# Performance work log

Hardware: AMD Instinct MI355X
Metric: run time of the kernel (lower is better)

The kernel has to match this reference:

```python
import jax, jax.numpy as jnp
import numpy as np

B, W, H, V, L = 64, 512, 1024, 32000, 2


def setup_inputs() -> dict:
    key = jax.random.key(0)
    ks = jax.random.split(key, 20)
    s = 0.02  # init scale
    n = lambda k, shp: jax.random.normal(k, shp, jnp.float32)
    return {
        "input": jax.random.randint(ks[0], (B, 1), 0, V),
        "h0": n(ks[1], (L, B, H)),
        "c0": n(ks[2], (L, B, H)),
        "encoder_output": n(ks[3], (B, W, H)),
        "embedding": n(ks[4], (V, H)) * s,
        "W_ih0": n(ks[5], (4 * H, H)) * s,
        "W_hh0": n(ks[6], (4 * H, H)) * s,
        "b_ih0": n(ks[7], (4 * H,)) * s,
        "b_hh0": n(ks[8], (4 * H,)) * s,
        "W_ih1": n(ks[9], (4 * H, H)) * s,
        "W_hh1": n(ks[10], (4 * H, H)) * s,
        "b_ih1": n(ks[11], (4 * H,)) * s,
        "b_hh1": n(ks[12], (4 * H,)) * s,
        "att_w": n(ks[13], (2 * H,)) * s,
        "att_b": n(ks[14], (1,)) * s,
        "input_W": n(ks[15], (H, 2 * H)) * s,
        "input_b": n(ks[16], (H,)) * s,
        "out_W": n(ks[17], (V, H)) * s,
        "out_b": n(ks[18], (V,)) * s,
    }


def _lstm_step(x, h, c, W_ih, W_hh, b_ih, b_hh):
    # PyTorch gate order: i, f, g, o
    g = x @ W_ih.T + h @ W_hh.T + b_ih + b_hh
    i, f, gg, o = jnp.split(g, 4, axis=-1)
    c2 = jax.nn.sigmoid(f) * c + jax.nn.sigmoid(i) * jnp.tanh(gg)
    return jax.nn.sigmoid(o) * jnp.tanh(c2), c2


def reference(input, h0, c0, encoder_output, embedding,
              W_ih0, W_hh0, b_ih0, b_hh0, W_ih1, W_hh1, b_ih1, b_hh1,
              att_w, att_b, input_W, input_b, out_W, out_b):
    Hd = h0.shape[-1]
    emb = embedding[input]                       # (B,1,H)
    att_state = h0[-1] * c0[-1]                  # (B,H)
    # Vectorized replacement of the per-word cat+linear loop:
    # att_line(cat(enc_w, att_state)) = enc_w @ w_enc + att_state @ w_st + b
    w_enc, w_st = att_w[:Hd], att_w[Hd:]
    scores = encoder_output @ w_enc + (att_state @ w_st)[:, None] + att_b[0]  # (B,W)
    # Original quirk: weigth starts with a zeros column, then softmax over
    # weigth[:, 0:-1] -> zero column + scores for words 0..W-2 (last dropped).
    zeros = jnp.zeros((scores.shape[0], 1), scores.dtype)
    full = jnp.concatenate([zeros, scores[:, :-1]], axis=1)  # (B,W)
    wts = jax.nn.softmax(full, axis=1)
    ctx = jnp.einsum('bw,bwh->bh', wts, encoder_output)      # (B,H)
    x = jnp.concatenate([ctx, emb[:, 0, :]], axis=-1)        # (B,2H)
    x = x @ input_W.T + input_b                              # (B,H)
    h1, c1 = _lstm_step(x, h0[0], c0[0], W_ih0, W_hh0, b_ih0, b_hh0)
    h2, c2 = _lstm_step(h1, h0[1], c0[1], W_ih1, W_hh1, b_ih1, b_hh1)
    logits = h2 @ out_W.T + out_b                            # (B,V)
    logp = jax.nn.log_softmax(logits, axis=-1)[:, None, :]   # (B,1,V)
    return logp, jnp.stack([h1, h2]), jnp.stack([c1, c2])
```

## Files before the change

kernel.cpp:

```cpp
#include <hip/hip_runtime.h>
#include <hip/hip_bf16.h>

#define Bsz 64
#define Wln 512
#define Hd  1024
#define Vc  32000

typedef short v8s __attribute__((ext_vector_type(8)));
typedef float f32x4 __attribute__((ext_vector_type(4)));

__device__ inline unsigned short f2b(float f) {
  union { float f; unsigned u; } v; v.f = f;
  return (unsigned short)((v.u + 0x8000u) >> 16);
}
__device__ inline float b2f(unsigned short u) {
  union { float f; unsigned u; } v; v.u = ((unsigned)u) << 16; return v.f;
}
__device__ inline float wave_sum(float v) {
  #pragma unroll
  for (int o = 32; o; o >>= 1) v += __shfl_down(v, o);
  return v;
}
__device__ inline float wave_max(float v) {
  #pragma unroll
  for (int o = 32; o; o >>= 1) v = fmaxf(v, __shfl_down(v, o));
  return v;
}
__device__ inline float wave_sum_all(float v) {
  #pragma unroll
  for (int o = 32; o; o >>= 1) v += __shfl_xor(v, o);
  return v;
}
__device__ inline float wave_max_all(float v) {
  #pragma unroll
  for (int o = 32; o; o >>= 1) v = fmaxf(v, __shfl_xor(v, o));
  return v;
}
__device__ inline float sigm(float x) { return 1.f / (1.f + expf(-x)); }

__device__ inline v8s cvt_frag(float4 x0, float4 x1) {
  v8s r;
  r[0] = (short)f2b(x0.x); r[1] = (short)f2b(x0.y);
  r[2] = (short)f2b(x0.z); r[3] = (short)f2b(x0.w);
  r[4] = (short)f2b(x1.x); r[5] = (short)f2b(x1.y);
  r[6] = (short)f2b(x1.z); r[7] = (short)f2b(x1.w);
  return r;
}

__device__ inline void stage_A(const float* __restrict__ A, const float* __restrict__ Ab,
                               int sA, char* pool, int tid) {
  #pragma unroll
  for (int it = 0; it < 16; ++it) {
    int idx = it * 512 + tid;
    int row = idx >> 7, ch = idx & 127;
    const float* src = A + (size_t)row * sA + ch * 8;
    float4 x0 = *(const float4*)src;
    float4 x1 = *(const float4*)(src + 4);
    if (Ab) {
      const float* s2 = Ab + (size_t)row * sA + ch * 8;
      float4 y0 = *(const float4*)s2;
      float4 y1 = *(const float4*)(s2 + 4);
      x0.x += y0.x; x0.y += y0.y; x0.z += y0.z; x0.w += y0.w;
      x1.x += y1.x; x1.y += y1.y; x1.z += y1.z; x1.w += y1.w;
    }
    *(v8s*)(pool + row * 2048 + ((ch * 16) ^ ((row & 7) << 4))) = cvt_frag(x0, x1);
  }
}

__global__ __launch_bounds__(512, 4) void k_attn(
    const float* __restrict__ enc, const float* __restrict__ att_w,
    const float* __restrict__ h0, const float* __restrict__ c0,
    const float* __restrict__ att_b,
    ushort* __restrict__ ctxp, float* __restrict__ ps_a)
{
  __shared__ __align__(16) float pool[8 * 1024];
  __shared__ float dots[17];
  __shared__ float redA[8];
  __shared__ float wts_sh[16];
  const int b = blockIdx.x >> 5, ch = blockIdx.x & 31;
  const int c0r = ch * 16;
  const int tid = threadIdx.x, w = tid >> 6, lane = tid & 63;
  const float* encb = enc + (size_t)b * Wln * Hd;

  const float* r0p = encb + (size_t)(c0r + 2 * w) * Hd;
  const float* r1p = r0p + Hd;
  float4 e0[4], e1[4], aw[4];
  #pragma unroll
  for (int i = 0; i < 4; ++i) {
    e0[i] = *(const float4*)(r0p + (i * 64 + lane) * 4);
    e1[i] = *(const float4*)(r1p + (i * 64 + lane) * 4);
    aw[i] = *(const float4*)(att_w + (i * 64 + lane) * 4);
  }

  {
    size_t base = (size_t)(Bsz + b) * Hd;
    int j = tid * 2;
    float s = h0[base + j] * c0[base + j] * att_w[Hd + j]
            + h0[base + j + 1] * c0[base + j + 1] * att_w[Hd + j + 1];
    s = wave_sum(s);
    if (lane == 0) redA[w] = s;
  }

  {
    float s0 = e0[0].x*aw[0].x + e0[0].y*aw[0].y + e0[0].z*aw[0].z + e0[0].w*aw[0].w
             + e0[1].x*aw[1].x + e0[1].y*aw[1].y + e0[1].z*aw[1].z + e0[1].w*aw[1].w
             + e0[2].x*aw[2].x + e0[2].y*aw[2].y + e0[2].z*aw[2].z + e0[2].w*aw[2].w
             + e0[3].x*aw[3].x + e0[3].y*aw[3].y + e0[3].z*aw[3].z + e0[3].w*aw[3].w;
    float s1 = e1[0].x*aw[0].x + e1[0].y*aw[0].y + e1[0].z*aw[0].z + e1[0].w*aw[0].w
             + e1[1].x*aw[1].x + e1[1].y*aw[1].y + e1[1].z*aw[1].z + e1[1].w*aw[1].w
             + e1[2].x*aw[2].x + e1[2].y*aw[2].y + e1[2].z*aw[2].z + e1[2].w*aw[2].w
             + e1[3].x*aw[3].x + e1[3].y*aw[3].y + e1[3].z*aw[3].z + e1[3].w*aw[3].w;
    s0 = wave_sum(s0);
    s1 = wave_sum(s1);
    if (lane == 0) { dots[2 * w + 1] = s0; dots[2 * w + 2] = s1; }
  }
  if (w == 7 && c0r > 0) {
    const float* hp = encb + (size_t)(c0r - 1) * Hd;
    float s = 0.f;
    #pragma unroll
    for (int i = 0; i < 4; ++i) {
      float4 hv = *(const float4*)(hp + (i * 64 + lane) * 4);
      s += hv.x*aw[i].x + hv.y*aw[i].y + hv.z*aw[i].z + hv.w*aw[i].w;
    }
    s = wave_sum(s);
    if (lane == 0) dots[0] = s;
  }
  __syncthreads();

  float sa = att_b[0];
  #pragma unroll
  for (int i = 0; i < 8; ++i) sa += redA[i];

  int r0 = c0r + 2 * w;
  float wt0 = (r0 == 0) ? 1.f : expf(dots[2 * w] + sa);
  float wt1 = expf(dots[2 * w + 1] + sa);
  if (lane == 0) { wts_sh[2 * w] = wt0; wts_sh[2 * w + 1] = wt1; }

  #pragma unroll
  for (int i = 0; i < 4; ++i) {
    float4 c4;
    c4.x = wt0 * e0[i].x + wt1 * e1[i].x;
    c4.y = wt0 * e0[i].y + wt1 * e1[i].y;
    c4.z = wt0 * e0[i].z + wt1 * e1[i].z;
    c4.w = wt0 * e0[i].w + wt1 * e1[i].w;
    *(float4*)(pool + w * 1024 + (i * 64 + lane) * 4) = c4;
  }
  __syncthreads();

  for (int c = tid; c < Hd; c += 512) {
    float s = 0.f;
    #pragma unroll
    for (int ww = 0; ww < 8; ++ww) s += pool[ww * 1024 + c];
    ctxp[(size_t)(b * 32 + ch) * Hd + c] = f2b(s);
  }
  if (tid == 0) {
    float S = 0.f;
    #pragma unroll
    for (int i = 0; i < 16; ++i) S += wts_sh[i];
    ps_a[b * 32 + ch] = S;
  }
}

__global__ __launch_bounds__(256) void k_ctx_fin(
    const ushort* __restrict__ ctxp, const float* __restrict__ ps_a,
    const int* __restrict__ input, const float* __restrict__ emb,
    float* __restrict__ cat)
{
  int b = blockIdx.x >> 2, qtr = blockIdx.x & 3;
  int t = threadIdx.x;
  float S = 0.f;
  #pragma unroll
  for (int c = 0; c < 32; ++c) S += ps_a[b * 32 + c];
  float inv = 1.f / S;
  int col = qtr * 256 + t;
  float s = 0.f;
  #pragma unroll 8
  for (int c = 0; c < 32; ++c) s += b2f(ctxp[(size_t)(b * 32 + c) * Hd + col]);
  cat[b * 2 * Hd + col] = s * inv;
  int idx = input[b];
  cat[b * 2 * Hd + Hd + col] = emb[(size_t)idx * Hd + col];
}

__global__ __launch_bounds__(512) void k_input_gemm(
    const float* __restrict__ cat, const float* __restrict__ inW,
    const float* __restrict__ inb, float* __restrict__ x1, float* __restrict__ x2)
{
  __shared__ __align__(16) char pool[131072];
  const int tid = threadIdx.x;
  const int w = tid >> 6, lane = tid & 63;
  const int r = lane & 15, q = lane >> 4;
  const int kh = w;
  const int half = (blockIdx.x >= 64);
  const int n0 = (blockIdx.x & 63) * 16;
  const float* A = cat + half * 1024;
  const float* B = inW + half * 1024;
  float* out = half ? x2 : x1;

  const float* bp = B + (size_t)(n0 + r) * 2048 + kh * 128 + q * 8;
  float4 breg[4][2];
  #pragma unroll
  for (int kk = 0; kk < 4; ++kk) {
    breg[kk][0] = *(const float4*)(bp + kk * 32);
    breg[kk][1] = *(const float4*)(bp + kk * 32 + 4);
  }
  stage_A(A, nullptr, 2048, pool, tid);
  __syncthreads();

  f32x4 acc[4] = {{0,0,0,0},{0,0,0,0},{0,0,0,0},{0,0,0,0}};
  const int swz = (r & 7) << 4;
  #pragma unroll
  for (int kk = 0; kk < 4; ++kk) {
    v8s bf = cvt_frag(breg[kk][0], breg[kk][1]);
    int cb = ((kh * 128 + kk * 32 + q * 8) * 2) ^ swz;
    #pragma unroll
    for (int m = 0; m < 4; ++m) {
      v8s af = *(const v8s*)(pool + (m * 16 + r) * 2048 + cb);
      acc[m] = __builtin_amdgcn_mfma_f32_16x16x32_bf16(af, bf, acc[m], 0, 0, 0);
    }
  }
  __syncthreads();

  float (*red)[64][17] = (float(*)[64][17])pool;
  #pragma unroll
  for (int m = 0; m < 4; ++m)
    #pragma unroll
    for (int rr = 0; rr < 4; ++rr)
      red[w][lane][m * 4 + rr] = acc[m][rr];
  __syncthreads();

  #pragma unroll
  for (int it = 0; it < 2; ++it) {
    int e = it * 512 + tid;
    int cc = e & 15, rowi = e >> 4;
    int idx = ((rowi >> 4) << 2) + (rowi & 3);
    int le  = (((rowi >> 2) & 3) << 4) + cc;
    float s = 0.f;
    #pragma unroll
    for (int j = 0; j < 8; ++j) s += red[j][le][idx];
    float bb = half ? 0.f : inb[n0 + cc];
    out[(size_t)rowi * Hd + n0 + cc] = s + bb;
  }
}

__global__ __launch_bounds__(512) void k_gate_lstm(
    const float* __restrict__ xA, const float* __restrict__ xAb,
    const float* __restrict__ hA,
    const float* __restrict__ W_ih, const float* __restrict__ W_hh,
    const float* __restrict__ b_ih, const float* __restrict__ b_hh,
    const float* __restrict__ c0,
    float* __restrict__ out_h, float* __restrict__ out_c)
{
  __shared__ __align__(16) char pool[131072];
  const int tid = threadIdx.x;
  const int w = tid >> 6, lane = tid & 63;
  const int r = lane & 15, q = lane >> 4;
  const int kh = w;
  const int gate = r >> 2, jl = r & 3;
  const size_t Brow = (size_t)gate * Hd + blockIdx.x * 4 + jl;

  float4 breg[2][4][2];
  {
    const float* bp0 = W_ih + Brow * Hd + kh * 128 + q * 8;
    const float* bp1 = W_hh + Brow * Hd + kh * 128 + q * 8;
    #pragma unroll
    for (int kk = 0; kk < 4; ++kk) {
      breg[0][kk][0] = *(const float4*)(bp0 + kk * 32);
      breg[0][kk][1] = *(const float4*)(bp0 + kk * 32 + 4);
      breg[1][kk][0] = *(const float4*)(bp1 + kk * 32);
      breg[1][kk][1] = *(const float4*)(bp1 + kk * 32 + 4);
    }
  }

  f32x4 acc[4] = {{0,0,0,0},{0,0,0,0},{0,0,0,0},{0,0,0,0}};
  const float* Amat[2] = { xA, hA };
  const float* Abm[2]  = { xAb, nullptr };
  #pragma unroll
  for (int p = 0; p < 2; ++p) {
    stage_A(Amat[p], Abm[p], Hd, pool, tid);
    __syncthreads();
    const int swz = (r & 7) << 4;
    #pragma unroll
    for (int kk = 0; kk < 4; ++kk) {
      v8s bf = cvt_frag(breg[p][kk][0], breg[p][kk][1]);
      int cb = ((kh * 128 + kk * 32 + q * 8) * 2) ^ swz;
      #pragma unroll
      for (int m = 0; m < 4; ++m) {
        v8s af = *(const v8s*)(pool + (m * 16 + r) * 2048 + cb);
        acc[m] = __builtin_amdgcn_mfma_f32_16x16x32_bf16(af, bf, acc[m], 0, 0, 0);
      }
    }
    __syncthreads();
  }

  float (*red)[64][17] = (float(*)[64][17])pool;
  #pragma unroll
  for (int m = 0; m < 4; ++m)
    #pragma unroll
    for (int rr = 0; rr < 4; ++rr)
      red[w][lane][m * 4 + rr] = acc[m][rr];
  __syncthreads();

  if (tid < 256) {
    int b = tid >> 2, jl2 = tid & 3;
    int jg = blockIdx.x * 4 + jl2;
    float gv[4];
    #pragma unroll
    for (int g2 = 0; g2 < 4; ++g2) {
      int cc = g2 * 4 + jl2;
      int idx = ((b >> 4) << 2) + (b & 3);
      int le  = (((b >> 2) & 3) << 4) + cc;
      float s = 0.f;
      #pragma unroll
      for (int j = 0; j < 8; ++j) s += red[j][le][idx];
      gv[g2] = s + b_ih[(size_t)g2 * Hd + jg] + b_hh[(size_t)g2 * Hd + jg];
    }
    float c = sigm(gv[1]) * c0[(size_t)b * Hd + jg] + sigm(gv[0]) * tanhf(gv[2]);
    float h = sigm(gv[3]) * tanhf(c);
    out_h[(size_t)b * Hd + jg] = h;
    out_c[(size_t)b * Hd + jg] = c;
  }
}

__global__ __launch_bounds__(512) void k_logits(
    const float* __restrict__ A, const float* __restrict__ B,
    const float* __restrict__ bias, float* __restrict__ out,
    float* __restrict__ pm, float* __restrict__ ps)
{
  __shared__ __align__(16) char pool[131072];
  const int tid = threadIdx.x;
  const int w = tid >> 6, lane = tid & 63;
  const int r = lane & 15, q = lane >> 4;
  const int nsub = w & 3, kh = w >> 2;
  const int n0 = blockIdx.x * 64;

  const float* bp = B + (size_t)(n0 + nsub * 16 + r) * Hd + kh * 512 + q * 8;
  float4 breg[16][2];
  #pragma unroll
  for (int kk = 0; kk < 16; ++kk) {
    breg[kk][0] = *(const float4*)(bp + kk * 32);
    breg[kk][1] = *(const float4*)(bp + kk * 32 + 4);
  }
  stage_A(A, nullptr, Hd, pool, tid);
  __syncthreads();

  f32x4 acc[4] = {{0,0,0,0},{0,0,0,0},{0,0,0,0},{0,0,0,0}};
  const int swz = (r & 7) << 4;
  #pragma unroll
  for (int kk = 0; kk < 16; ++kk) {
    v8s bf = cvt_frag(breg[kk][0], breg[kk][1]);
    int cb = ((kh * 512 + kk * 32 + q * 8) * 2) ^ swz;
    #pragma unroll
    for (int m = 0; m < 4; ++m) {
      v8s af = *(const v8s*)(pool + (m * 16 + r) * 2048 + cb);
      acc[m] = __builtin_amdgcn_mfma_f32_16x16x32_bf16(af, bf, acc[m], 0, 0, 0);
    }
  }
  __syncthreads();

  float (*red)[64][17] = (float(*)[64][17])pool;
  #pragma unroll
  for (int m = 0; m < 4; ++m)
    #pragma unroll
    for (int rr = 0; rr < 4; ++rr)
      red[w][lane][m * 4 + rr] = acc[m][rr];
  __syncthreads();

  #pragma unroll
  for (int it = 0; it < 8; ++it) {
    int e = it * 512 + tid;
    int cc = e & 63, rowi = e >> 6;
    int ns2 = cc >> 4, lo = cc & 15;
    int idx = ((rowi >> 4) << 2) + (rowi & 3);
    int le  = (((rowi >> 2) & 3) << 4) + lo;
    float val = red[ns2][le][idx] + red[ns2 + 4][le][idx] + bias[n0 + cc];
    out[(size_t)rowi * Vc + n0 + cc] = val;
    float wm = wave_max_all(val);
    float we = wave_sum_all(expf(val - wm));
    if (cc == 0) { pm[blockIdx.x * 64 + rowi] = wm; ps[blockIdx.x * 64 + rowi] = we; }
  }
}

__global__ __launch_bounds__(512) void k_lsm_sub(
    float* __restrict__ lg, const float* __restrict__ pm, const float* __restrict__ ps)
{
  __shared__ float redA[8], redB[8];
  int b = blockIdx.x >> 2, qc = blockIdx.x & 3;
  int tid = threadIdx.x, w = tid >> 6, lane = tid & 63;
  float m = -1e30f;
  for (int j = tid; j < 500; j += 512) m = fmaxf(m, pm[j * 64 + b]);
  m = wave_max(m);
  if (lane == 0) redA[w] = m;
  __syncthreads();
  float M = redA[0];
  #pragma unroll
  for (int i = 1; i < 8; ++i) M = fmaxf(M, redA[i]);
  float s = 0.f;
  for (int j = tid; j < 500; j += 512) s += ps[j * 64 + b] * expf(pm[j * 64 + b] - M);
  s = wave_sum(s);
  if (lane == 0) redB[w] = s;
  __syncthreads();
  float S = redB[0];
  #pragma unroll
  for (int i = 1; i < 8; ++i) S += redB[i];
  float lse = M + logf(S);
  float* row = lg + (size_t)b * Vc + qc * 8000;
  for (int j = tid * 4; j < 8000; j += 2048) {
    float4 v = *(const float4*)(row + j);
    v.x -= lse; v.y -= lse; v.z -= lse; v.w -= lse;
    *(float4*)(row + j) = v;
  }
}

extern "C" void kernel_launch(void* const* d_in, const int* in_sizes, int n_in,
                              void* d_out, int out_size, void* d_ws, size_t ws_size,
                              hipStream_t stream)
{
  const int*   input = (const int*)d_in[0];
  const float* h0    = (const float*)d_in[1];
  const float* c0    = (const float*)d_in[2];
  const float* enc   = (const float*)d_in[3];
  const float* emb   = (const float*)d_in[4];
  const float* W_ih0 = (const float*)d_in[5];
  const float* W_hh0 = (const float*)d_in[6];
  const float* b_ih0 = (const float*)d_in[7];
  const float* b_hh0 = (const float*)d_in[8];
  const float* W_ih1 = (const float*)d_in[9];
  const float* W_hh1 = (const float*)d_in[10];
  const float* b_ih1 = (const float*)d_in[11];
  const float* b_hh1 = (const float*)d_in[12];
  const float* att_w = (const float*)d_in[13];
  const float* att_b = (const float*)d_in[14];
  const float* inW   = (const float*)d_in[15];
  const float* inb   = (const float*)d_in[16];
  const float* outW  = (const float*)d_in[17];
  const float* outb  = (const float*)d_in[18];
  float* out = (float*)d_out;

  char* ws = (char*)d_ws;
  float*  cat  = (float*)(ws + 0);
  float*  x1   = (float*)(ws + 524288);
  float*  x2   = (float*)(ws + 786432);
  ushort* ctxp = (ushort*)(ws + 1048576);
  float*  ps_a = (float*)(ws + 5242880);
  float*  pm   = (float*)(ws + 5251072);
  float*  ps   = (float*)(ws + 5379072);

  float* out_h = out + (size_t)Bsz * Vc;
  float* out_c = out_h + 2 * Bsz * Hd;
  float* h1 = out_h;
  float* h2 = out_h + Bsz * Hd;

  k_attn<<<Bsz * 32, 512, 0, stream>>>(enc, att_w, h0, c0, att_b, ctxp, ps_a);
  k_ctx_fin<<<Bsz * 4, 256, 0, stream>>>(ctxp, ps_a, input, emb, cat);
  k_input_gemm<<<128, 512, 0, stream>>>(cat, inW, inb, x1, x2);
  k_gate_lstm<<<256, 512, 0, stream>>>(x1, x2, h0, W_ih0, W_hh0, b_ih0, b_hh0,
                                       c0, h1, out_c);
  k_gate_lstm<<<256, 512, 0, stream>>>(h1, nullptr, h0 + (size_t)Bsz * Hd,
                                       W_ih1, W_hh1, b_ih1, b_hh1,
                                       c0 + (size_t)Bsz * Hd, h2, out_c + Bsz * Hd);
  k_logits<<<500, 512, 0, stream>>>(h2, outW, outb, out, pm, ps);
  k_lsm_sub<<<256, 512, 0, stream>>>(out, pm, ps);
}
```

Measured before the change: 131.3 us.

## Precompute recurrent h@W_hh gate GEMMs inside attention kernel launch

The h0 @ W_hh^T products for both LSTM layers depend only on inputs, so they now run as 512 extra blocks appended to the attention kernel and write to workspace buffers. The gate kernels then do only the x @ W_ih^T half and add the precomputed recurrent term. This takes the W_hh weight streaming off the serial chain of dependent kernels and overlaps it with the attention work. In exchange it adds workspace traffic for two 64x4096 fp32 buffers, and the attention kernel now carries a larger register and LDS footprint.

```diff
diff --git a/kernel.cpp b/kernel.cpp
--- a/kernel.cpp
+++ b/kernel.cpp
@@ -71,93 +71,149 @@
     const float* __restrict__ enc, const float* __restrict__ att_w,
     const float* __restrict__ h0, const float* __restrict__ c0,
     const float* __restrict__ att_b,
-    ushort* __restrict__ ctxp, float* __restrict__ ps_a)
-{
-  __shared__ __align__(16) float pool[8 * 1024];
+    const float* __restrict__ W_hh0, const float* __restrict__ W_hh1,
+    ushort* __restrict__ ctxp, float* __restrict__ ps_a,
+    float* __restrict__ g2_0, float* __restrict__ g2_1)
+{
+  __shared__ __align__(16) char poolc[34816];
   __shared__ float dots[17];
   __shared__ float redA[8];
   __shared__ float wts_sh[16];
-  const int b = blockIdx.x >> 5, ch = blockIdx.x & 31;
-  const int c0r = ch * 16;
   const int tid = threadIdx.x, w = tid >> 6, lane = tid & 63;
-  const float* encb = enc + (size_t)b * Wln * Hd;
-
-  const float* r0p = encb + (size_t)(c0r + 2 * w) * Hd;
-  const float* r1p = r0p + Hd;
-  float4 e0[4], e1[4], aw[4];
-  #pragma unroll
-  for (int i = 0; i < 4; ++i) {
-    e0[i] = *(const float4*)(r0p + (i * 64 + lane) * 4);
-    e1[i] = *(const float4*)(r1p + (i * 64 + lane) * 4);
-    aw[i] = *(const float4*)(att_w + (i * 64 + lane) * 4);
-  }
-
-  {
-    size_t base = (size_t)(Bsz + b) * Hd;
-    int j = tid * 2;
-    float s = h0[base + j] * c0[base + j] * att_w[Hd + j]
-            + h0[base + j + 1] * c0[base + j + 1] * att_w[Hd + j + 1];
-    s = wave_sum(s);
-    if (lane == 0) redA[w] = s;
-  }
-
-  {
-    float s0 = e0[0].x*aw[0].x + e0[0].y*aw[0].y + e0[0].z*aw[0].z + e0[0].w*aw[0].w
-             + e0[1].x*aw[1].x + e0[1].y*aw[1].y + e0[1].z*aw[1].z + e0[1].w*aw[1].w
-             + e0[2].x*aw[2].x + e0[2].y*aw[2].y + e0[2].z*aw[2].z + e0[2].w*aw[2].w
-             + e0[3].x*aw[3].x + e0[3].y*aw[3].y + e0[3].z*aw[3].z + e0[3].w*aw[3].w;
-    float s1 = e1[0].x*aw[0].x + e1[0].y*aw[0].y + e1[0].z*aw[0].z + e1[0].w*aw[0].w
-             + e1[1].x*aw[1].x + e1[1].y*aw[1].y + e1[1].z*aw[1].z + e1[1].w*aw[1].w
-             + e1[2].x*aw[2].x + e1[2].y*aw[2].y + e1[2].z*aw[2].z + e1[2].w*aw[2].w
-             + e1[3].x*aw[3].x + e1[3].y*aw[3].y + e1[3].z*aw[3].z + e1[3].w*aw[3].w;
-    s0 = wave_sum(s0);
-    s1 = wave_sum(s1);
-    if (lane == 0) { dots[2 * w + 1] = s0; dots[2 * w + 2] = s1; }
-  }
-  if (w == 7 && c0r > 0) {
-    const float* hp = encb + (size_t)(c0r - 1) * Hd;
-    float s = 0.f;
+
+  if (blockIdx.x < 2048) {
+    float* pool = (float*)poolc;
+    const int b = blockIdx.x >> 5, ch = blockIdx.x & 31;
+    const int c0r = ch * 16;
+    const float* encb = enc + (size_t)b * Wln * Hd;
+
+    const float* r0p = encb + (size_t)(c0r + 2 * w) * Hd;
+    const float* r1p = r0p + Hd;
+    float4 e0[4], e1[4], aw[4];
     #pragma unroll
     for (int i = 0; i < 4; ++i) {
-      float4 hv = *(const float4*)(hp + (i * 64 + lane) * 4);
-      s += hv.x*aw[i].x + hv.y*aw[i].y + hv.z*aw[i].z + hv.w*aw[i].w;
-    }
-    s = wave_sum(s);
-    if (lane == 0) dots[0] = s;
-  }
-  __syncthreads();
-
-  float sa = att_b[0];
-  #pragma unroll
-  for (int i = 0; i < 8; ++i) sa += redA[i];
-
-  int r0 = c0r + 2 * w;
-  float wt0 = (r0 == 0) ? 1.f : expf(dots[2 * w] + sa);
-  float wt1 = expf(dots[2 * w + 1] + sa);
-  if (lane == 0) { wts_sh[2 * w] = wt0; wts_sh[2 * w + 1] = wt1; }
-
-  #pragma unroll
-  for (int i = 0; i < 4; ++i) {
-    float4 c4;
-    c4.x = wt0 * e0[i].x + wt1 * e1[i].x;
-    c4.y = wt0 * e0[i].y + wt1 * e1[i].y;
-    c4.z = wt0 * e0[i].z + wt1 * e1[i].z;
-    c4.w = wt0 * e0[i].w + wt1 * e1[i].w;
-    *(float4*)(pool + w * 1024 + (i * 64 + lane) * 4) = c4;
-  }
-  __syncthreads();
-
-  for (int c = tid; c < Hd; c += 512) {
-    float s = 0.f;
-    #pragma unroll
-    for (int ww = 0; ww < 8; ++ww) s += pool[ww * 1024 + c];
-    ctxp[(size_t)(b * 32 + ch) * Hd + c] = f2b(s);
-  }
-  if (tid == 0) {
-    float S = 0.f;
-    #pragma unroll
-    for (int i = 0; i < 16; ++i) S += wts_sh[i];
-    ps_a[b * 32 + ch] = S;
+      e0[i] = *(const float4*)(r0p + (i * 64 + lane) * 4);
+      e1[i] = *(const float4*)(r1p + (i * 64 + lane) * 4);
+      aw[i] = *(const float4*)(att_w + (i * 64 + lane) * 4);
+    }
+
+    {
+      size_t base = (size_t)(Bsz + b) * Hd;
+      int j = tid * 2;
+      float s = h0[base + j] * c0[base + j] * att_w[Hd + j]
+              + h0[base + j + 1] * c0[base + j + 1] * att_w[Hd + j + 1];
+      s = wave_sum(s);
+      if (lane == 0) redA[w] = s;
+    }
+
+    {
+      float s0 = e0[0].x*aw[0].x + e0[0].y*aw[0].y + e0[0].z*aw[0].z + e0[0].w*aw[0].w
+               + e0[1].x*aw[1].x + e0[1].y*aw[1].y + e0[1].z*aw[1].z + e0[1].w*aw[1].w
+               + e0[2].x*aw[2].x + e0[2].y*aw[2].y + e0[2].z*aw[2].z + e0[2].w*aw[2].w
+               + e0[3].x*aw[3].x + e0[3].y*aw[3].y + e0[3].z*aw[3].z + e0[3].w*aw[3].w;
+      float s1 = e1[0].x*aw[0].x + e1[0].y*aw[0].y + e1[0].z*aw[0].z + e1[0].w*aw[0].w
+               + e1[1].x*aw[1].x + e1[1].y*aw[1].y + e1[1].z*aw[1].z + e1[1].w*aw[1].w
+               + e1[2].x*aw[2].x + e1[2].y*aw[2].y + e1[2].z*aw[2].z + e1[2].w*aw[2].w
+               + e1[3].x*aw[3].x + e1[3].y*aw[3].y + e1[3].z*aw[3].z + e1[3].w*aw[3].w;
+      s0 = wave_sum(s0);
+      s1 = wave_sum(s1);
+      if (lane == 0) { dots[2 * w + 1] = s0; dots[2 * w + 2] = s1; }
+    }
+    if (w == 7 && c0r > 0) {
+      const float* hp = encb + (size_t)(c0r - 1) * Hd;
+      float s = 0.f;
+      #pragma unroll
+      for (int i = 0; i < 4; ++i) {
+        float4 hv = *(const float4*)(hp + (i * 64 + lane) * 4);
+        s += hv.x*aw[i].x + hv.y*aw[i].y + hv.z*aw[i].z + hv.w*aw[i].w;
+      }
+      s = wave_sum(s);
+      if (lane == 0) dots[0] = s;
+    }
+    __syncthreads();
+
+    float sa = att_b[0];
+    #pragma unroll
+    for (int i = 0; i < 8; ++i) sa += redA[i];
+
+    int r0 = c0r + 2 * w;
+    float wt0 = (r0 == 0) ? 1.f : expf(dots[2 * w] + sa);
+    float wt1 = expf(dots[2 * w + 1] + sa);
+    if (lane == 0) { wts_sh[2 * w] = wt0; wts_sh[2 * w + 1] = wt1; }
+
+    #pragma unroll
+    for (int i = 0; i < 4; ++i) {
+      float4 c4;
+      c4.x = wt0 * e0[i].x + wt1 * e1[i].x;
+      c4.y = wt0 * e0[i].y + wt1 * e1[i].y;
+      c4.z = wt0 * e0[i].z + wt1 * e1[i].z;
+      c4.w = wt0 * e0[i].w + wt1 * e1[i].w;
+      *(float4*)(pool + w * 1024 + (i * 64 + lane) * 4) = c4;
+    }
+    __syncthreads();
+
+    const int b32 = b * 32 + ch;
+    for (int c = tid; c < Hd; c += 512) {
+      float s = 0.f;
+      #pragma unroll
+      for (int ww = 0; ww < 8; ++ww) s += pool[ww * 1024 + c];
+      ctxp[(size_t)b32 * Hd + c] = f2b(s);
+    }
+    if (tid == 0) {
+      float S = 0.f;
+      #pragma unroll
+      for (int i = 0; i < 16; ++i) S += wts_sh[i];
+      ps_a[b32] = S;
+    }
+  } else {
+    int gb = blockIdx.x - 2048;
+    int layer = gb >> 8, blk = gb & 255;
+    const float* W  = layer ? W_hh1 : W_hh0;
+    const float* hA = h0 + (size_t)layer * Bsz * Hd;
+    float* g2o = layer ? g2_1 : g2_0;
+    const int n0 = blk * 16;
+    const int r = lane & 15, q = lane >> 4;
+    const int kh = w;
+
+    const float* bp = W + (size_t)(n0 + r) * Hd + kh * 128 + q * 8;
+    float4 breg[4][2];
+    #pragma unroll
+    for (int kk = 0; kk < 4; ++kk) {
+      breg[kk][0] = *(const float4*)(bp + kk * 32);
+      breg[kk][1] = *(const float4*)(bp + kk * 32 + 4);
+    }
+
+    f32x4 acc[4] = {{0,0,0,0},{0,0,0,0},{0,0,0,0},{0,0,0,0}};
+    #pragma unroll
+    for (int kk = 0; kk < 4; ++kk) {
+      v8s bf = cvt_frag(breg[kk][0], breg[kk][1]);
+      #pragma unroll
+      for (int m = 0; m < 4; ++m) {
+        const float* ap = hA + (size_t)(m * 16 + r) * Hd + kh * 128 + kk * 32 + q * 8;
+        v8s af = cvt_frag(*(const float4*)ap, *(const float4*)(ap + 4));
+        acc[m] = __builtin_amdgcn_mfma_f32_16x16x32_bf16(af, bf, acc[m], 0, 0, 0);
+      }
+    }
+
+    float (*red)[64][17] = (float(*)[64][17])poolc;
+    #pragma unroll
+    for (int m = 0; m < 4; ++m)
+      #pragma unroll
+      for (int rr = 0; rr < 4; ++rr)
+        red[w][lane][m * 4 + rr] = acc[m][rr];
+    __syncthreads();
+
+    #pragma unroll
+    for (int it = 0; it < 2; ++it) {
+      int e = it * 512 + tid;
+      int cc = e & 15, rowi = e >> 4;
+      int idx = ((rowi >> 4) << 2) + (rowi & 3);
+      int le  = (((rowi >> 2) & 3) << 4) + cc;
+      float s = 0.f;
+      #pragma unroll
+      for (int j = 0; j < 8; ++j) s += red[j][le][idx];
+      g2o[(size_t)rowi * 4096 + n0 + cc] = s;
+    }
   }
 }
 
@@ -244,8 +300,7 @@
 
 __global__ __launch_bounds__(512) void k_gate_lstm(
     const float* __restrict__ xA, const float* __restrict__ xAb,
-    const float* __restrict__ hA,
-    const float* __restrict__ W_ih, const float* __restrict__ W_hh,
+    const float* __restrict__ W_ih, const float* __restrict__ g2buf,
     const float* __restrict__ b_ih, const float* __restrict__ b_hh,
     const float* __restrict__ c0,
     float* __restrict__ out_h, float* __restrict__ out_c)
@@ -258,39 +313,29 @@
   const int gate = r >> 2, jl = r & 3;
   const size_t Brow = (size_t)gate * Hd + blockIdx.x * 4 + jl;
 
-  float4 breg[2][4][2];
-  {
-    const float* bp0 = W_ih + Brow * Hd + kh * 128 + q * 8;
-    const float* bp1 = W_hh + Brow * Hd + kh * 128 + q * 8;
-    #pragma unroll
-    for (int kk = 0; kk < 4; ++kk) {
-      breg[0][kk][0] = *(const float4*)(bp0 + kk * 32);
-      breg[0][kk][1] = *(const float4*)(bp0 + kk * 32 + 4);
-      breg[1][kk][0] = *(const float4*)(bp1 + kk * 32);
-      breg[1][kk][1] = *(const float4*)(bp1 + kk * 32 + 4);
-    }
-  }
+  const float* bp = W_ih + Brow * Hd + kh * 128 + q * 8;
+  float4 breg[4][2];
+  #pragma unroll
+  for (int kk = 0; kk < 4; ++kk) {
+    breg[kk][0] = *(const float4*)(bp + kk * 32);
+    breg[kk][1] = *(const float4*)(bp + kk * 32 + 4);
+  }
+  stage_A(xA, xAb, Hd, pool, tid);
+  __syncthreads();
 
   f32x4 acc[4] = {{0,0,0,0},{0,0,0,0},{0,0,0,0},{0,0,0,0}};
-  const float* Amat[2] = { xA, hA };
-  const float* Abm[2]  = { xAb, nullptr };
-  #pragma unroll
-  for (int p = 0; p < 2; ++p) {
-    stage_A(Amat[p], Abm[p], Hd, pool, tid);
-    __syncthreads();
-    const int swz = (r & 7) << 4;
-    #pragma unroll
-    for (int kk = 0; kk < 4; ++kk) {
-      v8s bf = cvt_frag(breg[p][kk][0], breg[p][kk][1]);
-      int cb = ((kh * 128 + kk * 32 + q * 8) * 2) ^ swz;
-      #pragma unroll
-      for (int m = 0; m < 4; ++m) {
-        v8s af = *(const v8s*)(pool + (m * 16 + r) * 2048 + cb);
-        acc[m] = __builtin_amdgcn_mfma_f32_16x16x32_bf16(af, bf, acc[m], 0, 0, 0);
-      }
-    }
-    __syncthreads();
-  }
+  const int swz = (r & 7) << 4;
+  #pragma unroll
+  for (int kk = 0; kk < 4; ++kk) {
+    v8s bf = cvt_frag(breg[kk][0], breg[kk][1]);
+    int cb = ((kh * 128 + kk * 32 + q * 8) * 2) ^ swz;
+    #pragma unroll
+    for (int m = 0; m < 4; ++m) {
+      v8s af = *(const v8s*)(pool + (m * 16 + r) * 2048 + cb);
+      acc[m] = __builtin_amdgcn_mfma_f32_16x16x32_bf16(af, bf, acc[m], 0, 0, 0);
+    }
+  }
+  __syncthreads();
 
   float (*red)[64][17] = (float(*)[64][17])pool;
   #pragma unroll
@@ -312,7 +357,8 @@
       float s = 0.f;
       #pragma unroll
       for (int j = 0; j < 8; ++j) s += red[j][le][idx];
-      gv[g2] = s + b_ih[(size_t)g2 * Hd + jg] + b_hh[(size_t)g2 * Hd + jg];
+      gv[g2] = s + g2buf[(size_t)b * 4096 + g2 * Hd + jg]
+                 + b_ih[(size_t)g2 * Hd + jg] + b_hh[(size_t)g2 * Hd + jg];
     }
     float c = sigm(gv[1]) * c0[(size_t)b * Hd + jg] + sigm(gv[0]) * tanhf(gv[2]);
     float h = sigm(gv[3]) * tanhf(c);
@@ -442,21 +488,23 @@
   float*  x2   = (float*)(ws + 786432);
   ushort* ctxp = (ushort*)(ws + 1048576);
   float*  ps_a = (float*)(ws + 5242880);
-  float*  pm   = (float*)(ws + 5251072);
-  float*  ps   = (float*)(ws + 5379072);
+  float*  g2_0 = (float*)(ws + 5251072);
+  float*  g2_1 = (float*)(ws + 6299648);
+  float*  pm   = (float*)(ws + 7348224);
+  float*  ps   = (float*)(ws + 7476224);
 
   float* out_h = out + (size_t)Bsz * Vc;
   float* out_c = out_h + 2 * Bsz * Hd;
   float* h1 = out_h;
   float* h2 = out_h + Bsz * Hd;
 
-  k_attn<<<Bsz * 32, 512, 0, stream>>>(enc, att_w, h0, c0, att_b, ctxp, ps_a);
+  k_attn<<<2560, 512, 0, stream>>>(enc, att_w, h0, c0, att_b, W_hh0, W_hh1,
+                                   ctxp, ps_a, g2_0, g2_1);
   k_ctx_fin<<<Bsz * 4, 256, 0, stream>>>(ctxp, ps_a, input, emb, cat);
   k_input_gemm<<<128, 512, 0, stream>>>(cat, inW, inb, x1, x2);
-  k_gate_lstm<<<256, 512, 0, stream>>>(x1, x2, h0, W_ih0, W_hh0, b_ih0, b_hh0,
+  k_gate_lstm<<<256, 512, 0, stream>>>(x1, x2, W_ih0, g2_0, b_ih0, b_hh0,
                                        c0, h1, out_c);
-  k_gate_lstm<<<256, 512, 0, stream>>>(h1, nullptr, h0 + (size_t)Bsz * Hd,
-                                       W_ih1, W_hh1, b_ih1, b_hh1,
+  k_gate_lstm<<<256, 512, 0, stream>>>(h1, nullptr, W_ih1, g2_1, b_ih1, b_hh1,
                                        c0 + (size_t)Bsz * Hd, h2, out_c + Bsz * Hd);
   k_logits<<<500, 512, 0, stream>>>(h2, outW, outb, out, pm, ps);
   k_lsm_sub<<<256, 512, 0, stream>>>(out, pm, ps);
```

After: 139.2 us. 5.9% more time.
